# Kernel optimization log

Measured on AMD Instinct MI355X. Metric: run time of the kernel, lower is better.

## Reference

```python
import jax, jax.numpy as jnp
import numpy as np

L = 2000          # per-modality dialogue length (all_dia_len)
M = 3             # num_modal
F = 512           # feature_size
E = 400000        # number of edges (<= 500000 edge_weight params)
N = M * L         # total nodes
NUM_LAYERS = 2
EW_SIZE = 500000
W_SCALE = 0.044   # ~1/sqrt(F) to keep activations sane


def setup_inputs() -> dict:
    key = jax.random.key(0)
    ks = jax.random.split(key, 9)
    x_a = jax.random.normal(ks[0], (L, F), jnp.float32)
    x_v = jax.random.normal(ks[1], (L, F), jnp.float32)
    x_t = jax.random.normal(ks[2], (L, F), jnp.float32)
    edge_index = jax.random.randint(ks[3], (2, E), 0, N, dtype=jnp.int32)
    edge_weight_param = jnp.ones((EW_SIZE,), jnp.float32)
    gcn_W = jax.random.normal(ks[4], (NUM_LAYERS, F, F), jnp.float32) * W_SCALE
    gcn_b = jnp.zeros((NUM_LAYERS, F), jnp.float32)
    fc_W = jax.random.normal(ks[5], (NUM_LAYERS, F, F), jnp.float32) * W_SCALE
    fc_b = jnp.zeros((NUM_LAYERS, F), jnp.float32)
    return {
        "x_a": x_a, "x_v": x_v, "x_t": x_t,
        "edge_weight_param": edge_weight_param,
        "gcn_W": gcn_W, "gcn_b": gcn_b,
        "fc_W": fc_W, "fc_b": fc_b,
        "edge_index": edge_index,
    }


def _gcn_fact(edge_index, edge_weight, num_nodes):
    # sparse edge list -> dense adjacency (scatter-add, duplicate edges coalesce)
    adj = jnp.zeros((num_nodes, num_nodes), edge_weight.dtype)
    adj = adj.at[edge_index[0], edge_index[1]].add(edge_weight)
    row_sum = adj.sum(axis=1)
    # torch: pow(row_sum, -0.5), inf -> 0  (safe form for zero-degree nodes)
    pos = row_sum > 0
    d_inv_sqrt = jnp.where(pos, jax.lax.rsqrt(jnp.where(pos, row_sum, 1.0)), 0.0)
    # D^{-1/2} A D^{-1/2} via row/col broadcast (same math as diag matmuls)
    return d_inv_sqrt[:, None] * adj * d_inv_sqrt[None, :]


def reference(x_a, x_v, x_t, edge_weight_param, gcn_W, gcn_b, fc_W, fc_b, edge_index):
    feature = jnp.concatenate([x_a, x_v, x_t], axis=0)      # [N, F]
    edge_weight = edge_weight_param[: edge_index.shape[1]]   # [E]
    gcn = _gcn_fact(edge_index, edge_weight, feature.shape[0])
    feature_sum = feature
    for i in range(NUM_LAYERS):
        # encoder layer: one dense GCN propagation + projection
        feature = jax.nn.relu(gcn @ feature @ gcn_W[i] + gcn_b[i])
        # fc layer: Linear + LeakyReLU (dropout = identity at eval)
        feature_sum = feature_sum + jax.nn.leaky_relu(feature @ fc_W[i] + fc_b[i], 0.01)
    # chunk back into per-modality features
    return tuple(jnp.split(feature_sum, M, axis=0))
```

## Files before the change

kernel.cpp:

```cpp
#include <hip/hip_runtime.h>
#include <hip/hip_bf16.h>

#define LL 2000
#define MM 3
#define FF 512
#define NN (MM * LL)
#define NUM_LAYERS 2
#define CAP 128

typedef __attribute__((ext_vector_type(8))) short bf16x8;
typedef __attribute__((ext_vector_type(4))) float f32x4;

__device__ __forceinline__ unsigned short f2bf(float x) {
    __hip_bfloat16 b = __float2bfloat16(x);
    return *(unsigned short*)&b;
}

__device__ __forceinline__ void gload16(const void* gsrc, void* ldst) {
    __builtin_amdgcn_global_load_lds((const __attribute__((address_space(1))) unsigned int*)gsrc,
                                     (__attribute__((address_space(3))) unsigned int*)ldst,
                                     16, 0, 0);
}

__global__ __launch_bounds__(256) void prep(const float* __restrict__ xa,
                                            const float* __restrict__ xv,
                                            const float* __restrict__ xt,
                                            unsigned short* __restrict__ feat,
                                            float* __restrict__ out_sum,
                                            const float* __restrict__ gcnW,
                                            const float* __restrict__ fcW,
                                            unsigned short* __restrict__ Wt,
                                            const int* __restrict__ esrc,
                                            int* __restrict__ counts,
                                            int* __restrict__ pir, int E) {
    __shared__ unsigned short tile[64][65];
    int b = blockIdx.x;
    int tid = threadIdx.x;
    if (b < 3000) {
        int idx4 = b * 256 + tid;
        const int per4 = (LL * FF) / 4;
        const float4* src;
        int off;
        if (idx4 < per4)            { src = (const float4*)xa; off = idx4; }
        else if (idx4 < 2 * per4)   { src = (const float4*)xv; off = idx4 - per4; }
        else                        { src = (const float4*)xt; off = idx4 - 2 * per4; }
        float4 v = src[off];
        ((float4*)out_sum)[idx4] = v;
        ushort4 pk;
        pk.x = f2bf(v.x); pk.y = f2bf(v.y); pk.z = f2bf(v.z); pk.w = f2bf(v.w);
        ((ushort4*)feat)[idx4] = pk;
    } else if (b < 3256) {
        int idx = b - 3000;
        int mz = idx >> 6;
        int rem = idx & 63;
        int k0 = (rem >> 3) * 64;
        int n0 = (rem & 7) * 64;
        int layer = (mz < 2) ? mz : mz - 2;
        const float* src = (mz < 2) ? (gcnW + (size_t)layer * FF * FF)
                                    : (fcW + (size_t)layer * FF * FF);
        int slot = (mz < 2) ? (mz * 2) : ((mz - 2) * 2 + 1);
        unsigned short* dst = Wt + (size_t)slot * FF * FF;
        for (int i = tid; i < 64 * 64; i += 256) {
            int r = i >> 6, c = i & 63;
            tile[r][c] = f2bf(src[(size_t)(k0 + r) * FF + n0 + c]);
        }
        __syncthreads();
        for (int i = tid; i < 64 * 64; i += 256) {
            int r = i >> 6, c = i & 63;
            dst[(size_t)(n0 + r) * FF + k0 + c] = tile[c][r];
        }
    } else {
        int e = (b - 3256) * 256 + tid;
        if (e < E) pir[e] = atomicAdd(&counts[esrc[e]], 1);
    }
}

__global__ __launch_bounds__(256) void gemm0_scatter(const unsigned short* __restrict__ A,
                                                     const unsigned short* __restrict__ Bt,
                                                     unsigned short* __restrict__ Hout,
                                                     int M, int gxm, int ngemm,
                                                     const int* __restrict__ esrc,
                                                     const int* __restrict__ edst,
                                                     const float* __restrict__ ew,
                                                     const int* __restrict__ pir,
                                                     int2* __restrict__ bucket, int E) {
    __shared__ short As[64 * 64];
    __shared__ short Bs[64 * 64];
    int b = blockIdx.x;
    int tid = threadIdx.x;
    if (b >= ngemm) {
        int e = (b - ngemm) * 256 + tid;
        if (e < E) {
            int r = esrc[e];
            int slot = pir[e];
            if (slot < CAP) {
                int2 p;
                p.x = edst[e];
                p.y = __float_as_int(ew[e]);
                bucket[(size_t)r * CAP + slot] = p;
            }
        }
        return;
    }
    int wave = tid >> 6;
    int lane = tid & 63;
    int lane16 = lane & 15;
    int quad = lane >> 4;
    int m0 = (b % gxm) * 64;
    int n0 = (b / gxm) * 64;
    int wm = (wave >> 1) * 32;
    int wn = (wave & 1) * 32;

    f32x4 acc[2][2] = {};

    for (int k0 = 0; k0 < FF; k0 += 64) {
#pragma unroll
        for (int s = 0; s < 2; s++) {
            int c = wave * 128 + s * 64 + lane;
            int row = c >> 3;
            int kc = (c & 7) ^ (row & 7);
            int ar = m0 + row; if (ar >= M) ar = M - 1;
            gload16((const short*)A + (size_t)ar * FF + k0 + kc * 8,
                    &As[(wave * 128 + s * 64) * 8]);
            gload16((const short*)Bt + (size_t)(n0 + row) * FF + k0 + kc * 8,
                    &Bs[(wave * 128 + s * 64) * 8]);
        }
        __syncthreads();
#pragma unroll
        for (int kk = 0; kk < 2; kk++) {
            bf16x8 a[2], bb[2];
#pragma unroll
            for (int mt = 0; mt < 2; mt++) {
                int row = wm + mt * 16 + lane16;
                int kc = (kk * 4 + quad) ^ (row & 7);
                a[mt] = *(const bf16x8*)&As[row * 64 + kc * 8];
            }
#pragma unroll
            for (int nt = 0; nt < 2; nt++) {
                int row = wn + nt * 16 + lane16;
                int kc = (kk * 4 + quad) ^ (row & 7);
                bb[nt] = *(const bf16x8*)&Bs[row * 64 + kc * 8];
            }
#pragma unroll
            for (int mt = 0; mt < 2; mt++)
#pragma unroll
                for (int nt = 0; nt < 2; nt++)
                    acc[mt][nt] = __builtin_amdgcn_mfma_f32_16x16x32_bf16(a[mt], bb[nt], acc[mt][nt], 0, 0, 0);
        }
        __syncthreads();
    }

#pragma unroll
    for (int mt = 0; mt < 2; mt++) {
#pragma unroll
        for (int nt = 0; nt < 2; nt++) {
            int n = n0 + wn + nt * 16 + lane16;
#pragma unroll
            for (int rr = 0; rr < 4; rr++) {
                int m = m0 + wm + mt * 16 + quad * 4 + rr;
                if (m < M) Hout[(size_t)m * FF + n] = f2bf(acc[mt][nt][rr]);
            }
        }
    }
}

__global__ __launch_bounds__(256) void rowsum_dinv(const int2* __restrict__ bucket,
                                                   const int* __restrict__ counts,
                                                   float* __restrict__ dinv) {
    int wave = threadIdx.x >> 6, lane = threadIdx.x & 63;
    int r = blockIdx.x * 4 + wave;
    int s = r * CAP;
    int e = s + min(counts[r], CAP);
    float sum = 0.0f;
    for (int i = s + lane; i < e; i += 64) sum += __int_as_float(bucket[i].y);
#pragma unroll
    for (int off = 32; off > 0; off >>= 1) sum += __shfl_xor(sum, off);
    if (lane == 0) dinv[r] = (sum > 0.0f) ? rsqrtf(sum) : 0.0f;
}

__device__ __forceinline__ void accum8(float* acc, uint4 h, float v) {
    unsigned int d[4] = {h.x, h.y, h.z, h.w};
#pragma unroll
    for (int k = 0; k < 4; k++) {
        float lo = __uint_as_float(d[k] << 16);
        float hi = __uint_as_float(d[k] & 0xFFFF0000u);
        acc[2 * k]     = fmaf(v, lo, acc[2 * k]);
        acc[2 * k + 1] = fmaf(v, hi, acc[2 * k + 1]);
    }
}

__global__ __launch_bounds__(256) void spmm_bias_relu(const unsigned short* __restrict__ H,
                                                      const int* __restrict__ counts,
                                                      const int2* __restrict__ bucket,
                                                      const float* __restrict__ dinv,
                                                      const float* __restrict__ bias,
                                                      unsigned short* __restrict__ featOut) {
    int wave = threadIdx.x >> 6, lane = threadIdx.x & 63;
    int r = blockIdx.x * 4 + wave;
    int s = r * CAP;
    int e = s + min(counts[r], CAP);
    int f0 = lane * 8;
    const unsigned short* Hf = H + f0;
    float acc[8] = {0, 0, 0, 0, 0, 0, 0, 0};

    int i = s;
    int2 p0, p1, p2, p3;
    bool have = (i + 4 <= e);
    if (have) { p0 = bucket[i]; p1 = bucket[i + 1]; p2 = bucket[i + 2]; p3 = bucket[i + 3]; }
    while (have) {
        uint4 a0 = *(const uint4*)(Hf + (size_t)p0.x * FF);
        uint4 a1 = *(const uint4*)(Hf + (size_t)p1.x * FF);
        uint4 a2 = *(const uint4*)(Hf + (size_t)p2.x * FF);
        uint4 a3 = *(const uint4*)(Hf + (size_t)p3.x * FF);
        float v0 = __int_as_float(p0.y) * dinv[p0.x];
        float v1 = __int_as_float(p1.y) * dinv[p1.x];
        float v2 = __int_as_float(p2.y) * dinv[p2.x];
        float v3 = __int_as_float(p3.y) * dinv[p3.x];
        i += 4;
        have = (i + 4 <= e);
        if (have) { p0 = bucket[i]; p1 = bucket[i + 1]; p2 = bucket[i + 2]; p3 = bucket[i + 3]; }
        accum8(acc, a0, v0);
        accum8(acc, a1, v1);
        accum8(acc, a2, v2);
        accum8(acc, a3, v3);
    }
    for (; i < e; i++) {
        int2 p = bucket[i];
        uint4 a = *(const uint4*)(Hf + (size_t)p.x * FF);
        accum8(acc, a, __int_as_float(p.y) * dinv[p.x]);
    }

    float dr = dinv[r];
    float4 b0 = *(const float4*)(bias + f0);
    float4 b1 = *(const float4*)(bias + f0 + 4);
    float bb[8] = {b0.x, b0.y, b0.z, b0.w, b1.x, b1.y, b1.z, b1.w};
    unsigned int o[4];
#pragma unroll
    for (int k = 0; k < 4; k++) {
        float v0 = fmaxf(fmaf(acc[2 * k], dr, bb[2 * k]), 0.0f);
        float v1 = fmaxf(fmaf(acc[2 * k + 1], dr, bb[2 * k + 1]), 0.0f);
        o[k] = (unsigned int)f2bf(v0) | ((unsigned int)f2bf(v1) << 16);
    }
    uint4 ov; ov.x = o[0]; ov.y = o[1]; ov.z = o[2]; ov.w = o[3];
    *(uint4*)(featOut + (size_t)r * FF + f0) = ov;
}

template <int MODE>
__global__ __launch_bounds__(256) void gemm_bf16(const unsigned short* __restrict__ A,
                                                 const unsigned short* __restrict__ Bt,
                                                 const float* __restrict__ fbias,
                                                 unsigned short* __restrict__ Hout,
                                                 float* __restrict__ out,
                                                 int M) {
    __shared__ short As[64 * 64];
    __shared__ short Bs[64 * 64];
    int tid = threadIdx.x;
    int wave = tid >> 6;
    int lane = tid & 63;
    int lane16 = lane & 15;
    int quad = lane >> 4;
    int m0 = blockIdx.x * 64;
    int n0 = blockIdx.y * 64;
    int wm = (wave >> 1) * 32;
    int wn = (wave & 1) * 32;

    f32x4 acc[2][2] = {};

    for (int k0 = 0; k0 < FF; k0 += 64) {
#pragma unroll
        for (int s = 0; s < 2; s++) {
            int c = wave * 128 + s * 64 + lane;
            int row = c >> 3;
            int kc = (c & 7) ^ (row & 7);
            int ar = m0 + row; if (ar >= M) ar = M - 1;
            gload16((const short*)A + (size_t)ar * FF + k0 + kc * 8,
                    &As[(wave * 128 + s * 64) * 8]);
            gload16((const short*)Bt + (size_t)(n0 + row) * FF + k0 + kc * 8,
                    &Bs[(wave * 128 + s * 64) * 8]);
        }
        __syncthreads();
#pragma unroll
        for (int kk = 0; kk < 2; kk++) {
            bf16x8 a[2], bb[2];
#pragma unroll
            for (int mt = 0; mt < 2; mt++) {
                int row = wm + mt * 16 + lane16;
                int kc = (kk * 4 + quad) ^ (row & 7);
                a[mt] = *(const bf16x8*)&As[row * 64 + kc * 8];
            }
#pragma unroll
            for (int nt = 0; nt < 2; nt++) {
                int row = wn + nt * 16 + lane16;
                int kc = (kk * 4 + quad) ^ (row & 7);
                bb[nt] = *(const bf16x8*)&Bs[row * 64 + kc * 8];
            }
#pragma unroll
            for (int mt = 0; mt < 2; mt++)
#pragma unroll
                for (int nt = 0; nt < 2; nt++)
                    acc[mt][nt] = __builtin_amdgcn_mfma_f32_16x16x32_bf16(a[mt], bb[nt], acc[mt][nt], 0, 0, 0);
        }
        __syncthreads();
    }

    bool isFc = (MODE == 1) || (MODE == 2 && n0 < FF);
#pragma unroll
    for (int mt = 0; mt < 2; mt++) {
#pragma unroll
        for (int nt = 0; nt < 2; nt++) {
            int n = n0 + wn + nt * 16 + lane16;
            float bv = isFc ? fbias[n] : 0.0f;
#pragma unroll
            for (int rr = 0; rr < 4; rr++) {
                int m = m0 + wm + mt * 16 + quad * 4 + rr;
                if (m < M) {
                    float v = acc[mt][nt][rr];
                    if (isFc) {
                        v += bv;
                        v = (v > 0.0f) ? v : 0.01f * v;
                        out[(size_t)m * FF + n] += v;
                    } else {
                        Hout[(size_t)m * FF + (n - FF)] = f2bf(v);
                    }
                }
            }
        }
    }
}

extern "C" void kernel_launch(void* const* d_in, const int* in_sizes, int n_in,
                              void* d_out, int out_size, void* d_ws, size_t ws_size,
                              hipStream_t stream) {
    const float* xa      = (const float*)d_in[0];
    const float* xv      = (const float*)d_in[1];
    const float* xt      = (const float*)d_in[2];
    const float* ew      = (const float*)d_in[3];
    const float* gcn_W   = (const float*)d_in[4];
    const float* gcn_b   = (const float*)d_in[5];
    const float* fc_W    = (const float*)d_in[6];
    const float* fc_b    = (const float*)d_in[7];
    const int*   eidx    = (const int*)d_in[8];
    const int E = in_sizes[8] / 2;
    const int* esrc = eidx;
    const int* edst = eidx + E;

    float* out = (float*)d_out;

    char* w = (char*)d_ws;
    int*   counts  = (int*)  (w + 0);
    float* dinv    = (float*)(w + 24064);
    int2*  bucket  = (int2*) (w + 48128);
    unsigned short* feat = (unsigned short*)(w + 6192128);
    unsigned short* H    = (unsigned short*)(w + 12336128);
    unsigned short* Wt   = (unsigned short*)(w + 18480128);
    int*   pir     = (int*)  (w + 20577280);

    hipMemsetAsync(counts, 0, 24000, stream);

    const int eblocks = (E + 255) / 256;
    prep<<<3256 + eblocks, 256, 0, stream>>>(xa, xv, xt, feat, out,
                                             gcn_W, fc_W, Wt, esrc, counts, pir, E);

    const int gxm = (NN + 63) / 64;
    const int ngemm0 = gxm * 8;
    gemm0_scatter<<<ngemm0 + eblocks, 256, 0, stream>>>(feat, Wt, H, NN, gxm, ngemm0,
                                                        esrc, edst, ew, pir, bucket, E);
    rowsum_dinv<<<NN / 4, 256, 0, stream>>>(bucket, counts, dinv);

    spmm_bias_relu<<<NN / 4, 256, 0, stream>>>(H, counts, bucket, dinv, gcn_b, feat);
    gemm_bf16<2><<<dim3(gxm, 16), 256, 0, stream>>>(feat, Wt + (size_t)FF * FF, fc_b, H, out, NN);
    spmm_bias_relu<<<NN / 4, 256, 0, stream>>>(H, counts, bucket, dinv, gcn_b + FF, feat);
    gemm_bf16<1><<<dim3(gxm, 8), 256, 0, stream>>>(feat, Wt + (size_t)3 * FF * FF, fc_b + FF, nullptr, out, NN);
}
```

Before: 210.1 us.

## Co-schedule layer-0 fc GEMM with layer-1 SpMM in one launch

The combined layer-0 fc and layer-1 GCN projection GEMM is split in two. The gcn projection runs first to produce H, then a single fused launch runs the fc GEMM blocks alongside the layer-1 SpMM rows. A second feature buffer avoids a read/write conflict between them. The edge-scatter blocks in gemm0_scatter are also moved to the front of the grid so they dispatch first. This is meant to overlap the latency-bound gather SpMM with the compute-bound GEMM, at the cost of one extra launch and an extra workspace buffer.

```diff
diff --git a/kernel.cpp b/kernel.cpp
--- a/kernel.cpp
+++ b/kernel.cpp
@@ -78,7 +78,7 @@
 __global__ __launch_bounds__(256) void gemm0_scatter(const unsigned short* __restrict__ A,
                                                      const unsigned short* __restrict__ Bt,
                                                      unsigned short* __restrict__ Hout,
-                                                     int M, int gxm, int ngemm,
+                                                     int M, int gxm, int sblk,
                                                      const int* __restrict__ esrc,
                                                      const int* __restrict__ edst,
                                                      const float* __restrict__ ew,
@@ -88,8 +88,8 @@
     __shared__ short Bs[64 * 64];
     int b = blockIdx.x;
     int tid = threadIdx.x;
-    if (b >= ngemm) {
-        int e = (b - ngemm) * 256 + tid;
+    if (b < sblk) {
+        int e = b * 256 + tid;
         if (e < E) {
             int r = esrc[e];
             int slot = pir[e];
@@ -102,12 +102,13 @@
         }
         return;
     }
+    int bg = b - sblk;
     int wave = tid >> 6;
     int lane = tid & 63;
     int lane16 = lane & 15;
     int quad = lane >> 4;
-    int m0 = (b % gxm) * 64;
-    int n0 = (b / gxm) * 64;
+    int m0 = (bg % gxm) * 64;
+    int n0 = (bg / gxm) * 64;
     int wm = (wave >> 1) * 32;
     int wn = (wave & 1) * 32;
 
@@ -189,14 +190,13 @@
     }
 }
 
-__global__ __launch_bounds__(256) void spmm_bias_relu(const unsigned short* __restrict__ H,
-                                                      const int* __restrict__ counts,
-                                                      const int2* __restrict__ bucket,
-                                                      const float* __restrict__ dinv,
-                                                      const float* __restrict__ bias,
-                                                      unsigned short* __restrict__ featOut) {
-    int wave = threadIdx.x >> 6, lane = threadIdx.x & 63;
-    int r = blockIdx.x * 4 + wave;
+__device__ __forceinline__ void spmm_row(const unsigned short* __restrict__ H,
+                                         const int* __restrict__ counts,
+                                         const int2* __restrict__ bucket,
+                                         const float* __restrict__ dinv,
+                                         const float* __restrict__ bias,
+                                         unsigned short* __restrict__ featOut,
+                                         int r, int lane) {
     int s = r * CAP;
     int e = s + min(counts[r], CAP);
     int f0 = lane * 8;
@@ -245,6 +245,17 @@
     *(uint4*)(featOut + (size_t)r * FF + f0) = ov;
 }
 
+__global__ __launch_bounds__(256) void spmm_bias_relu(const unsigned short* __restrict__ H,
+                                                      const int* __restrict__ counts,
+                                                      const int2* __restrict__ bucket,
+                                                      const float* __restrict__ dinv,
+                                                      const float* __restrict__ bias,
+                                                      unsigned short* __restrict__ featOut) {
+    int wave = threadIdx.x >> 6, lane = threadIdx.x & 63;
+    int r = blockIdx.x * 4 + wave;
+    spmm_row(H, counts, bucket, dinv, bias, featOut, r, lane);
+}
+
 template <int MODE>
 __global__ __launch_bounds__(256) void gemm_bf16(const unsigned short* __restrict__ A,
                                                  const unsigned short* __restrict__ Bt,
@@ -303,25 +314,111 @@
         __syncthreads();
     }
 
-    bool isFc = (MODE == 1) || (MODE == 2 && n0 < FF);
 #pragma unroll
     for (int mt = 0; mt < 2; mt++) {
 #pragma unroll
         for (int nt = 0; nt < 2; nt++) {
             int n = n0 + wn + nt * 16 + lane16;
-            float bv = isFc ? fbias[n] : 0.0f;
+            float bv = (MODE == 1) ? fbias[n] : 0.0f;
 #pragma unroll
             for (int rr = 0; rr < 4; rr++) {
                 int m = m0 + wm + mt * 16 + quad * 4 + rr;
                 if (m < M) {
                     float v = acc[mt][nt][rr];
-                    if (isFc) {
+                    if (MODE == 1) {
                         v += bv;
                         v = (v > 0.0f) ? v : 0.01f * v;
                         out[(size_t)m * FF + n] += v;
                     } else {
-                        Hout[(size_t)m * FF + (n - FF)] = f2bf(v);
+                        Hout[(size_t)m * FF + n] = f2bf(v);
                     }
+                }
+            }
+        }
+    }
+}
+
+__global__ __launch_bounds__(256) void fc_spmm(const unsigned short* __restrict__ A,
+                                               const unsigned short* __restrict__ Bt,
+                                               const float* __restrict__ fbias,
+                                               float* __restrict__ out,
+                                               int M, int gxm, int ngemm,
+                                               const unsigned short* __restrict__ H,
+                                               const int* __restrict__ counts,
+                                               const int2* __restrict__ bucket,
+                                               const float* __restrict__ dinv,
+                                               const float* __restrict__ bias,
+                                               unsigned short* __restrict__ featOut) {
+    __shared__ short As[64 * 64];
+    __shared__ short Bs[64 * 64];
+    int b = blockIdx.x;
+    int tid = threadIdx.x;
+    int wave = tid >> 6;
+    int lane = tid & 63;
+    if (b >= ngemm) {
+        int r = (b - ngemm) * 4 + wave;
+        spmm_row(H, counts, bucket, dinv, bias, featOut, r, lane);
+        return;
+    }
+    int lane16 = lane & 15;
+    int quad = lane >> 4;
+    int m0 = (b % gxm) * 64;
+    int n0 = (b / gxm) * 64;
+    int wm = (wave >> 1) * 32;
+    int wn = (wave & 1) * 32;
+
+    f32x4 acc[2][2] = {};
+
+    for (int k0 = 0; k0 < FF; k0 += 64) {
+#pragma unroll
+        for (int s = 0; s < 2; s++) {
+            int c = wave * 128 + s * 64 + lane;
+            int row = c >> 3;
+            int kc = (c & 7) ^ (row & 7);
+            int ar = m0 + row; if (ar >= M) ar = M - 1;
+            gload16((const short*)A + (size_t)ar * FF + k0 + kc * 8,
+                    &As[(wave * 128 + s * 64) * 8]);
+            gload16((const short*)Bt + (size_t)(n0 + row) * FF + k0 + kc * 8,
+                    &Bs[(wave * 128 + s * 64) * 8]);
+        }
+        __syncthreads();
+#pragma unroll
+        for (int kk = 0; kk < 2; kk++) {
+            bf16x8 a[2], bb[2];
+#pragma unroll
+            for (int mt = 0; mt < 2; mt++) {
+                int row = wm + mt * 16 + lane16;
+                int kc = (kk * 4 + quad) ^ (row & 7);
+                a[mt] = *(const bf16x8*)&As[row * 64 + kc * 8];
+            }
+#pragma unroll
+            for (int nt = 0; nt < 2; nt++) {
+                int row = wn + nt * 16 + lane16;
+                int kc = (kk * 4 + quad) ^ (row & 7);
+                bb[nt] = *(const bf16x8*)&Bs[row * 64 + kc * 8];
+            }
+#pragma unroll
+            for (int mt = 0; mt < 2; mt++)
+#pragma unroll
+                for (int nt = 0; nt < 2; nt++)
+                    acc[mt][nt] = __builtin_amdgcn_mfma_f32_16x16x32_bf16(a[mt], bb[nt], acc[mt][nt], 0, 0, 0);
+        }
+        __syncthreads();
+    }
+
+#pragma unroll
+    for (int mt = 0; mt < 2; mt++) {
+#pragma unroll
+        for (int nt = 0; nt < 2; nt++) {
+            int n = n0 + wn + nt * 16 + lane16;
+            float bv = fbias[n];
+#pragma unroll
+            for (int rr = 0; rr < 4; rr++) {
+                int m = m0 + wm + mt * 16 + quad * 4 + rr;
+                if (m < M) {
+                    float v = acc[mt][nt][rr] + bv;
+                    v = (v > 0.0f) ? v : 0.01f * v;
+                    out[(size_t)m * FF + n] += v;
                 }
             }
         }
@@ -350,25 +447,30 @@
     int*   counts  = (int*)  (w + 0);
     float* dinv    = (float*)(w + 24064);
     int2*  bucket  = (int2*) (w + 48128);
-    unsigned short* feat = (unsigned short*)(w + 6192128);
-    unsigned short* H    = (unsigned short*)(w + 12336128);
-    unsigned short* Wt   = (unsigned short*)(w + 18480128);
-    int*   pir     = (int*)  (w + 20577280);
+    unsigned short* featA = (unsigned short*)(w + 6192128);
+    unsigned short* featB = (unsigned short*)(w + 12336128);
+    unsigned short* H     = (unsigned short*)(w + 18480128);
+    unsigned short* Wt    = (unsigned short*)(w + 24624128);
+    int*   pir     = (int*)  (w + 26721280);
 
     hipMemsetAsync(counts, 0, 24000, stream);
 
     const int eblocks = (E + 255) / 256;
-    prep<<<3256 + eblocks, 256, 0, stream>>>(xa, xv, xt, feat, out,
+    prep<<<3256 + eblocks, 256, 0, stream>>>(xa, xv, xt, featA, out,
                                              gcn_W, fc_W, Wt, esrc, counts, pir, E);
 
     const int gxm = (NN + 63) / 64;
-    const int ngemm0 = gxm * 8;
-    gemm0_scatter<<<ngemm0 + eblocks, 256, 0, stream>>>(feat, Wt, H, NN, gxm, ngemm0,
-                                                        esrc, edst, ew, pir, bucket, E);
+    const int ngemm = gxm * 8;
+    gemm0_scatter<<<eblocks + ngemm, 256, 0, stream>>>(featA, Wt, H, NN, gxm, eblocks,
+                                                       esrc, edst, ew, pir, bucket, E);
     rowsum_dinv<<<NN / 4, 256, 0, stream>>>(bucket, counts, dinv);
 
-    spmm_bias_relu<<<NN / 4, 256, 0, stream>>>(H, counts, bucket, dinv, gcn_b, feat);
-    gemm_bf16<2><<<dim3(gxm, 16), 256, 0, stream>>>(feat, Wt + (size_t)FF * FF, fc_b, H, out, NN);
-    spmm_bias_relu<<<NN / 4, 256, 0, stream>>>(H, counts, bucket, dinv, gcn_b + FF, feat);
-    gemm_bf16<1><<<dim3(gxm, 8), 256, 0, stream>>>(feat, Wt + (size_t)3 * FF * FF, fc_b + FF, nullptr, out, NN);
-}
+    spmm_bias_relu<<<NN / 4, 256, 0, stream>>>(H, counts, bucket, dinv, gcn_b, featA);
+    gemm_bf16<0><<<dim3(gxm, 8), 256, 0, stream>>>(featA, Wt + (size_t)2 * FF * FF,
+                                                   nullptr, H, nullptr, NN);
+    fc_spmm<<<ngemm + NN / 4, 256, 0, stream>>>(featA, Wt + (size_t)FF * FF, fc_b,
+                                                out, NN, gxm, ngemm,
+                                                H, counts, bucket, dinv, gcn_b + FF, featB);
+    gemm_bf16<1><<<dim3(gxm, 8), 256, 0, stream>>>(featB, Wt + (size_t)3 * FF * FF,
+                                                   fc_b + FF, nullptr, out, NN);
+}
```

After: 219.1 us. 4.3% more time.
